# Kernel optimization log

Measured on AMD Instinct MI355X. Metric: run time of the kernel, lower is better.

The kernel has to match this reference:

```python
import jax, jax.numpy as jnp
import numpy as np

K = 7  # local_kernel_size


def conv2d(x, w, b, pad):
    # x: [B,C,H,W], w: [O,I,kh,kw]
    y = jax.lax.conv_general_dilated(
        x, w, window_strides=(1, 1), padding=[(pad, pad), (pad, pad)],
        dimension_numbers=("NCHW", "OIHW", "NCHW"))
    return y + b[None, :, None, None]


def kernel_normalize(kernel, k):
    # kernel: [B, k*k, H, W]; zero-mean over tap dim, then add 1/(k*k)
    km = jnp.mean(kernel, axis=1, keepdims=True)
    return kernel - km + 1.0 / (k * k)


def local_conv_feat(img, kernel, k):
    # Fused dynamic local conv: avoids materializing [B,C,k*k,H,W].
    # Tap order matches F.unfold row-major (dy, dx).
    B, C, H, W = img.shape
    pad = (k - 1) // 2
    imgp = jnp.pad(img, ((0, 0), (0, 0), (pad, pad), (pad, pad)))
    out = jnp.zeros_like(img)
    for dy in range(k):
        for dx in range(k):
            idx = dy * k + dx
            out = out + imgp[:, :, dy:dy + H, dx:dx + W] * kernel[:, idx:idx + 1]
    return out


def setup_inputs() -> dict:
    key = jax.random.key(0)
    ks = jax.random.split(key, 14)
    B, C, H, W = 4, 64, 128, 128
    w = lambda k, shape: jax.random.normal(k, shape, jnp.float32) * 0.05
    return {
        "x": jax.random.normal(ks[0], (B, C, H, W), jnp.float32),
        "kernel_features": jax.random.normal(ks[1], (B, C, H, W), jnp.float32),
        # feature_path: two 3x3 convs
        "fw1": w(ks[2], (C, C, 3, 3)), "fb1": jnp.zeros((C,), jnp.float32),
        "fw2": w(ks[3], (C, C, 3, 3)), "fb2": jnp.zeros((C,), jnp.float32),
        # multiplicative_path: two 3x3 convs
        "mw1": w(ks[4], (C, C, 3, 3)), "mb1": jnp.zeros((C,), jnp.float32),
        "mw2": w(ks[5], (C, C, 3, 3)), "mb2": jnp.zeros((C,), jnp.float32),
        # local_filter_path: two 1x1 convs, last outputs k*k channels
        "lw1": w(ks[6], (C, C, 1, 1)), "lb1": jnp.zeros((C,), jnp.float32),
        "lw2": w(ks[7], (K * K, C, 1, 1)), "lb2": jnp.zeros((K * K,), jnp.float32),
    }


def reference(x, kernel_features, fw1, fb1, fw2, fb2, mw1, mb1, mw2, mb2, lw1, lb1, lw2, lb2):
    # feature_path: ReLU -> conv3x3 -> ReLU -> conv3x3
    fp = conv2d(jax.nn.relu(conv2d(jax.nn.relu(x), fw1, fb1, 1)), fw2, fb2, 1)
    # multiplicative_path: conv3x3 -> ReLU -> conv3x3
    mp = conv2d(jax.nn.relu(conv2d(kernel_features, mw1, mb1, 1)), mw2, mb2, 1)
    # local_filter_path: conv1x1 -> ReLU -> conv1x1 (-> k*k channels)
    lp = conv2d(jax.nn.relu(conv2d(kernel_features, lw1, lb1, 0)), lw2, lb2, 0)
    lp = kernel_normalize(lp, K)
    feat = fp * mp
    filtered = local_conv_feat(feat, lp, K)
    return x + filtered
```

## Files before the change

kernel.cpp:

```cpp
#include <hip/hip_runtime.h>
#include <hip/hip_bf16.h>

#define Cc 64
#define Hc 128
#define Wc 128
#define HWc (Hc * Wc)
#define Bc 4

typedef __attribute__((ext_vector_type(8))) short short8;
typedef __attribute__((ext_vector_type(4))) float float4v;

static __device__ __forceinline__ unsigned short f2bu(float f) {
    __hip_bfloat16 h = __float2bfloat16(f);
    return *(unsigned short*)&h;
}
static __device__ __forceinline__ float bulo(unsigned int u) {
    return __uint_as_float((u & 0xffffu) << 16);
}
static __device__ __forceinline__ float buhi(unsigned int u) {
    return __uint_as_float(u & 0xffff0000u);
}

static __device__ __forceinline__ void gl_lds16(const void* g, void* l) {
    __builtin_amdgcn_global_load_lds(
        (const __attribute__((address_space(1))) unsigned int*)g,
        (__attribute__((address_space(3))) unsigned int*)l, 16, 0, 0);
}

__global__ __launch_bounds__(256) void prep_k(
    const float* __restrict__ x, const float* __restrict__ kf,
    const float* __restrict__ fw1, const float* __restrict__ fw2,
    const float* __restrict__ mw1, const float* __restrict__ mw2,
    const float* __restrict__ lw1, const float* __restrict__ lw2,
    unsigned short* __restrict__ xb, unsigned short* __restrict__ kfb,
    unsigned short* __restrict__ wbase, unsigned short* __restrict__ zpage)
{
    const int bid = blockIdx.x;
    const int tid = threadIdx.x;

    if (bid < 512) {
        const bool isx = bid < 256;
        const float* src = isx ? x : kf;
        unsigned short* dst = isx ? xb : kfb;
        const int px = (isx ? bid : bid - 256) * 256 + tid;
        const int b  = px >> 14;
        const int hw = px & 16383;
        const float* s = src + (size_t)b * Cc * HWc + hw;
        unsigned short* d = dst + (size_t)px * Cc;
#pragma unroll
        for (int c8 = 0; c8 < 8; ++c8) {
            unsigned int pk[4];
#pragma unroll
            for (int jp = 0; jp < 4; ++jp) {
                float v0 = s[(size_t)(c8 * 8 + jp * 2 + 0) * HWc];
                float v1 = s[(size_t)(c8 * 8 + jp * 2 + 1) * HWc];
                if (isx) { v0 = fmaxf(v0, 0.f); v1 = fmaxf(v1, 0.f); }
                pk[jp] = (unsigned int)f2bu(v0) | ((unsigned int)f2bu(v1) << 16);
            }
            *(uint4*)(d + c8 * 8) = make_uint4(pk[0], pk[1], pk[2], pk[3]);
        }
    } else if (bid < 584) {
        const int wbid  = bid - 512;
        const int which = wbid / 18;
        const float* w = (which == 0) ? fw1 : (which == 1) ? fw2 : (which == 2) ? mw1 : mw2;
        unsigned short* wb = wbase + (size_t)which * 36864;
        const int g = (wbid % 18) * 256 + tid;
        if (g >= 4608) return;
        const int lane = g & 63;
        const int smt  = g >> 6;
        const int s    = smt >> 2;
        const int mt   = smt & 3;
        const int co   = mt * 16 + (lane & 15);
        const int kb   = s * 32 + (lane >> 4) * 8;
        unsigned int pk[4];
#pragma unroll
        for (int jp = 0; jp < 4; ++jp) {
            int k0 = kb + jp * 2, k1 = k0 + 1;
            float v0 = w[((size_t)co * Cc + (k0 & 63)) * 9 + (k0 >> 6)];
            float v1 = w[((size_t)co * Cc + (k1 & 63)) * 9 + (k1 >> 6)];
            pk[jp] = (unsigned int)f2bu(v0) | ((unsigned int)f2bu(v1) << 16);
        }
        *(uint4*)(wb + (size_t)g * 8) = make_uint4(pk[0], pk[1], pk[2], pk[3]);
    } else if (bid < 588) {
        const int wbid  = bid - 584;
        const int which = wbid >> 1;
        const float* w = which ? lw2 : lw1;
        const int Cout = which ? 49 : 64;
        unsigned short* wb = wbase + 4 * 36864 + (size_t)which * 4096;
        const int g = (wbid & 1) * 256 + tid;
        const int lane = g & 63;
        const int smt  = g >> 6;
        const int s    = smt >> 2;
        const int mt   = smt & 3;
        const int co   = mt * 16 + (lane & 15);
        const int kb   = s * 32 + (lane >> 4) * 8;
        unsigned int pk[4];
#pragma unroll
        for (int jp = 0; jp < 4; ++jp) {
            int k0 = kb + jp * 2, k1 = k0 + 1;
            float v0 = (co < Cout) ? w[(size_t)co * Cc + k0] : 0.f;
            float v1 = (co < Cout) ? w[(size_t)co * Cc + k1] : 0.f;
            pk[jp] = (unsigned int)f2bu(v0) | ((unsigned int)f2bu(v1) << 16);
        }
        *(uint4*)(wb + (size_t)g * 8) = make_uint4(pk[0], pk[1], pk[2], pk[3]);
    } else {
        if (tid < 64) ((unsigned int*)zpage)[tid] = 0;
    }
}

#define STAGE_DMA(INPTR, SBUF)                                                \
    for (int k = wv; k < 33; k += 4) {                                        \
        const int u_  = k * 8 + (lane >> 3);                                  \
        const int j_  = lane & 7;                                             \
        const int r_  = u_ / 66;                                              \
        const int c_  = u_ - r_ * 66;                                         \
        const int gh_ = h0 - 1 + r_;                                          \
        const int gw_ = w0 - 1 + c_;                                          \
        const bool ok_ = ((unsigned)gh_ < (unsigned)Hc) && ((unsigned)gw_ < (unsigned)Wc); \
        const int ch_ = j_ ^ (u_ & 7);                                        \
        const unsigned short* g_ = ok_                                        \
            ? (INPTR) + ((((size_t)b * Hc + gh_) * Wc + gw_) << 6) + (ch_ << 3) \
            : zpage + (ch_ << 3);                                             \
        gl_lds16(g_, &(SBUF)[k * 512]);                                       \
    }

#define LOAD_A(W, s, m) (*(const short8*)((W) + (size_t)(s) * 2048 + (size_t)(m) * 512))
#define LOAD_B(SB, s, nt) ({                                                  \
        const int tap_ = (s) >> 1;                                            \
        const int qb_  = rowb[tap_ / 3] + tap_ % 3;                           \
        const int ch0_ = ((s) & 1) * 4 + quad;                                \
        *(const short8*)&(SB)[(qb_ + (nt) * 16) * 64 + ((ch0_ ^ (qb_ & 7)) << 3)]; })

#define CONV_GEMM(APTR, ACC, SB)                                              \
    {                                                                         \
        short8 a_buf[4][2], b_cur[4], b_nxt[4];                               \
        _Pragma("unroll")                                                     \
        for (int q = 0; q < 3; ++q)                                           \
            _Pragma("unroll")                                                 \
            for (int m = 0; m < 2; ++m) a_buf[q][m] = LOAD_A(APTR, q, m);     \
        _Pragma("unroll")                                                     \
        for (int nt = 0; nt < 4; ++nt) b_cur[nt] = LOAD_B(SB, 0, nt);         \
        _Pragma("unroll")                                                     \
        for (int s = 0; s < 18; ++s) {                                        \
            if (s + 3 < 18) {                                                 \
                _Pragma("unroll")                                             \
                for (int m = 0; m < 2; ++m)                                   \
                    a_buf[(s + 3) & 3][m] = LOAD_A(APTR, s + 3, m);           \
            }                                                                 \
            if (s + 1 < 18) {                                                 \
                _Pragma("unroll")                                             \
                for (int nt = 0; nt < 4; ++nt)                                \
                    b_nxt[nt] = LOAD_B(SB, s + 1, nt);                        \
            }                                                                 \
            _Pragma("unroll")                                                 \
            for (int nt = 0; nt < 4; ++nt)                                    \
                _Pragma("unroll")                                             \
                for (int m = 0; m < 2; ++m)                                   \
                    ACC[m][nt] = __builtin_amdgcn_mfma_f32_16x16x32_bf16(     \
                        a_buf[s & 3][m], b_cur[nt], ACC[m][nt], 0, 0, 0);     \
            if (s + 1 < 18) {                                                 \
                _Pragma("unroll")                                             \
                for (int nt = 0; nt < 4; ++nt) b_cur[nt] = b_nxt[nt];         \
            }                                                                 \
        }                                                                     \
    }

__global__ __launch_bounds__(256) void conv1_lp_k(
    const unsigned short* __restrict__ in0,
    const unsigned short* __restrict__ in1,
    const unsigned short* __restrict__ wfrag0,
    const unsigned short* __restrict__ wfrag1,
    const float* __restrict__ bias0,
    const float* __restrict__ bias1,
    const unsigned short* __restrict__ zpage,
    unsigned short* __restrict__ out0,
    unsigned short* __restrict__ out1,
    const unsigned short* __restrict__ w1, const float* __restrict__ b1,
    const unsigned short* __restrict__ w2, const float* __restrict__ b2,
    unsigned short* __restrict__ lpout)
{
    __shared__ unsigned short s_b[264 * 64];

    const int tid  = threadIdx.x;
    const int lane = tid & 63;
    const int wv   = tid >> 6;
    const int quad = lane >> 4;
    const int glin = blockIdx.x;
    const int xcd  = glin & 7;
    const int slot = glin >> 3;

    if (slot < 128) {
        const int sel = slot >> 6;
        const int hti = slot & 63;
        const int b   = xcd >> 1;
        const int w0  = (xcd & 1) * 64;
        const int h0  = hti * 2;

        const unsigned short* in    = sel ? in1 : in0;
        const unsigned short* wfrag = sel ? wfrag1 : wfrag0;
        const float*          bias  = sel ? bias1 : bias0;
        unsigned short*       out   = sel ? out1 : out0;

        STAGE_DMA(in, s_b);
        __syncthreads();

        const int rowsel = wv >> 1;
        const int cohalf = wv & 1;
        const int n15    = lane & 15;
        const unsigned short* aptr = wfrag + (((size_t)(cohalf * 2) * 64 + lane) << 3);

        int rowb[3];
#pragma unroll
        for (int ky = 0; ky < 3; ++ky) rowb[ky] = (rowsel + ky) * 66 + n15;

        float4v acc[2][4];
#pragma unroll
        for (int m = 0; m < 2; ++m)
#pragma unroll
            for (int nt = 0; nt < 4; ++nt) acc[m][nt] = (float4v){0.f, 0.f, 0.f, 0.f};

        CONV_GEMM(aptr, acc, s_b);

        const int h = h0 + rowsel;
#pragma unroll
        for (int m = 0; m < 2; ++m) {
            const int mt  = cohalf * 2 + m;
            const int co0 = mt * 16 + quad * 4;
            float4 bv = *(const float4*)&bias[co0];
#pragma unroll
            for (int nt = 0; nt < 4; ++nt) {
                const size_t pix = ((size_t)b * Hc + h) * Wc + w0 + nt * 16 + n15;
                ushort4 pk;
                pk.x = f2bu(fmaxf(acc[m][nt][0] + bv.x, 0.f));
                pk.y = f2bu(fmaxf(acc[m][nt][1] + bv.y, 0.f));
                pk.z = f2bu(fmaxf(acc[m][nt][2] + bv.z, 0.f));
                pk.w = f2bu(fmaxf(acc[m][nt][3] + bv.w, 0.f));
                *(ushort4*)&out[pix * Cc + co0] = pk;
            }
        }
    } else {
        const int lpid = xcd * 128 + (slot - 128);
        const int p    = lane & 15;
        const size_t pix = (size_t)lpid * 64 + wv * 16 + p;
        unsigned short* st = &s_b[wv * 1024];

        float4v acc1[4];
#pragma unroll
        for (int mt = 0; mt < 4; ++mt) acc1[mt] = (float4v){0.f, 0.f, 0.f, 0.f};
#pragma unroll
        for (int s = 0; s < 2; ++s) {
            short8 bfr = *(const short8*)&in1[pix * Cc + s * 32 + quad * 8];
#pragma unroll
            for (int mt = 0; mt < 4; ++mt) {
                short8 afr = *(const short8*)&w1[(size_t)(((s * 4 + mt) << 6) + lane) << 3];
                acc1[mt] = __builtin_amdgcn_mfma_f32_16x16x32_bf16(afr, bfr, acc1[mt], 0, 0, 0);
            }
        }

#pragma unroll
        for (int mt = 0; mt < 4; ++mt) {
            const int co0 = mt * 16 + quad * 4;
            float4 bv = *(const float4*)&b1[co0];
            ushort4 pk;
            pk.x = f2bu(fmaxf(acc1[mt][0] + bv.x, 0.f));
            pk.y = f2bu(fmaxf(acc1[mt][1] + bv.y, 0.f));
            pk.z = f2bu(fmaxf(acc1[mt][2] + bv.z, 0.f));
            pk.w = f2bu(fmaxf(acc1[mt][3] + bv.w, 0.f));
            const int cg = co0 >> 3;
            *(ushort4*)&st[p * 64 + ((cg ^ (p & 7)) << 3) + (quad & 1) * 4] = pk;
        }
        __syncthreads();

        float4v acc2[4];
#pragma unroll
        for (int mt = 0; mt < 4; ++mt) acc2[mt] = (float4v){0.f, 0.f, 0.f, 0.f};
#pragma unroll
        for (int s = 0; s < 2; ++s) {
            const int cg = s * 4 + quad;
            short8 bfr = *(const short8*)&st[p * 64 + ((cg ^ (p & 7)) << 3)];
#pragma unroll
            for (int mt = 0; mt < 4; ++mt) {
                short8 afr = *(const short8*)&w2[(size_t)(((s * 4 + mt) << 6) + lane) << 3];
                acc2[mt] = __builtin_amdgcn_mfma_f32_16x16x32_bf16(afr, bfr, acc2[mt], 0, 0, 0);
            }
        }

        float v[4][4];
        float partial = 0.f;
#pragma unroll
        for (int mt = 0; mt < 4; ++mt) {
#pragma unroll
            for (int r = 0; r < 4; ++r) {
                const int tap = mt * 16 + quad * 4 + r;
                float val = (tap < 49) ? (acc2[mt][r] + b2[tap]) : 0.f;
                v[mt][r] = val;
                partial += val;
            }
        }
        partial += __shfl_xor(partial, 16, 64);
        partial += __shfl_xor(partial, 32, 64);
        const float m = partial * (1.f / 49.f) - (1.f / 49.f);

        const int b  = (int)(pix >> 14);
        const int hw = (int)(pix & 16383);
#pragma unroll
        for (int mt = 0; mt < 4; ++mt) {
#pragma unroll
            for (int r = 0; r < 4; ++r) {
                const int tap = mt * 16 + quad * 4 + r;
                if (tap < 49)
                    lpout[((size_t)b * 49 + tap) * HWc + hw] = f2bu(v[mt][r] - m);
            }
        }
    }
}

__global__ __launch_bounds__(256) void conv2_fused_k(
    const unsigned short* __restrict__ t1f,
    const unsigned short* __restrict__ t1m,
    const unsigned short* __restrict__ wf,
    const unsigned short* __restrict__ wm,
    const float* __restrict__ bf,
    const float* __restrict__ bm,
    const unsigned short* __restrict__ zpage,
    unsigned short* __restrict__ featp)
{
    __shared__ unsigned short s_b2[2][264 * 64];

    const int tid  = threadIdx.x;
    const int lane = tid & 63;
    const int wv   = tid >> 6;
    const int glin = blockIdx.x;
    const int xcd  = glin & 7;
    const int slot = glin >> 3;
    const int b    = xcd >> 1;
    const int w0   = (xcd & 1) * 64;
    const int h0   = slot * 2;

    STAGE_DMA(t1f, s_b2[0]);
    STAGE_DMA(t1m, s_b2[1]);
    __syncthreads();

    const int rowsel = wv >> 1;
    const int cohalf = wv & 1;
    const int quad   = lane >> 4;
    const int n15    = lane & 15;

    int rowb[3];
#pragma unroll
    for (int ky = 0; ky < 3; ++ky) rowb[ky] = (rowsel + ky) * 66 + n15;

    float4v acc[2][4];
#pragma unroll
    for (int m = 0; m < 2; ++m)
#pragma unroll
        for (int nt = 0; nt < 4; ++nt) acc[m][nt] = (float4v){0.f, 0.f, 0.f, 0.f};

    {
        const unsigned short* aptr = wf + (((size_t)(cohalf * 2) * 64 + lane) << 3);
        CONV_GEMM(aptr, acc, s_b2[0]);
    }

    float fpv[2][4][4];
#pragma unroll
    for (int m = 0; m < 2; ++m) {
        const int mt  = cohalf * 2 + m;
        const int co0 = mt * 16 + quad * 4;
        float4 bv = *(const float4*)&bf[co0];
#pragma unroll
        for (int nt = 0; nt < 4; ++nt) {
            fpv[m][nt][0] = bulo((unsigned int)f2bu(acc[m][nt][0] + bv.x));
            fpv[m][nt][1] = bulo((unsigned int)f2bu(acc[m][nt][1] + bv.y));
            fpv[m][nt][2] = bulo((unsigned int)f2bu(acc[m][nt][2] + bv.z));
            fpv[m][nt][3] = bulo((unsigned int)f2bu(acc[m][nt][3] + bv.w));
        }
    }

#pragma unroll
    for (int m = 0; m < 2; ++m)
#pragma unroll
        for (int nt = 0; nt < 4; ++nt) acc[m][nt] = (float4v){0.f, 0.f, 0.f, 0.f};

    {
        const unsigned short* aptr = wm + (((size_t)(cohalf * 2) * 64 + lane) << 3);
        CONV_GEMM(aptr, acc, s_b2[1]);
    }

    const int h = h0 + rowsel;
#pragma unroll
    for (int m = 0; m < 2; ++m) {
        const int mt  = cohalf * 2 + m;
        const int co0 = mt * 16 + quad * 4;
        float4 bv = *(const float4*)&bm[co0];
#pragma unroll
        for (int nt = 0; nt < 4; ++nt) {
            const int px = h * Wc + w0 + nt * 16 + n15;
            float v[4] = {acc[m][nt][0] + bv.x, acc[m][nt][1] + bv.y,
                          acc[m][nt][2] + bv.z, acc[m][nt][3] + bv.w};
#pragma unroll
            for (int r = 0; r < 4; ++r)
                featp[((size_t)b * Cc + co0 + r) * HWc + px] =
                    f2bu(v[r] * fpv[m][nt][r]);
        }
    }
}

__global__ __launch_bounds__(256) void local_conv_v4(
    const float* __restrict__ x, const unsigned short* __restrict__ featp,
    const unsigned short* __restrict__ lp, float* __restrict__ out)
{
    const int tid  = threadIdx.x;
    const int glin = blockIdx.x;
    const int xcd  = glin & 7;
    const int slot = glin >> 3;
    const int pair = xcd * 8 + (slot >> 4);
    const int cg   = slot & 15;
    const int b    = pair >> 4;
    const int hti  = pair & 15;

    const int w4  = (tid & 31) * 4;
    const int ro  = tid >> 5;
    const int h   = hti * 8 + ro;
    const int c0  = cg * 4;

    float msk[12];
#pragma unroll
    for (int e = 0; e < 12; ++e) {
        int gw = w4 - 4 + e;
        msk[e] = ((unsigned)gw < (unsigned)Wc) ? 1.f : 0.f;
    }

    float acc[4][4];
#pragma unroll
    for (int ch = 0; ch < 4; ++ch)
#pragma unroll
        for (int p = 0; p < 4; ++p) acc[ch][p] = 0.f;

    const unsigned short* lpb = lp + (size_t)b * 49 * HWc + (size_t)h * Wc + w4;
    const unsigned short* fb  = featp + ((size_t)b * Cc + c0) * HWc;

#pragma unroll
    for (int dy = 0; dy < 7; ++dy) {
        const int gh = h + dy - 3;
        if ((unsigned)gh >= (unsigned)Hc) continue;

        float lpf[7][4];
#pragma unroll
        for (int dx = 0; dx < 7; ++dx) {
            uint2 lv = *(const uint2*)&lpb[(size_t)(dy * 7 + dx) * HWc];
            lpf[dx][0] = bulo(lv.x); lpf[dx][1] = buhi(lv.x);
            lpf[dx][2] = bulo(lv.y); lpf[dx][3] = buhi(lv.y);
        }

        const unsigned short* frow = fb + (size_t)gh * Wc + w4;
#pragma unroll
        for (int ch = 0; ch < 4; ++ch) {
            const unsigned short* fr = frow + (size_t)ch * HWc;
            uint2 a  = *(const uint2*)(fr - 4);
            uint2 bq = *(const uint2*)(fr);
            uint2 cq = *(const uint2*)(fr + 4);
            float f[12];
            f[0]  = bulo(a.x);             f[1]  = buhi(a.x) * msk[1];
            f[2]  = bulo(a.y) * msk[2];    f[3]  = buhi(a.y) * msk[3];
            f[4]  = bulo(bq.x);            f[5]  = buhi(bq.x);
            f[6]  = bulo(bq.y);            f[7]  = buhi(bq.y);
            f[8]  = bulo(cq.x) * msk[8];   f[9]  = buhi(cq.x) * msk[9];
            f[10] = bulo(cq.y) * msk[10];  f[11] = buhi(cq.y);
#pragma unroll
            for (int dx = 0; dx < 7; ++dx)
#pragma unroll
                for (int p = 0; p < 4; ++p)
                    acc[ch][p] = fmaf(f[p + dx + 1], lpf[dx][p], acc[ch][p]);
        }
    }

#pragma unroll
    for (int ch = 0; ch < 4; ++ch) {
        const size_t idx = ((size_t)b * Cc + c0 + ch) * HWc + (size_t)h * Wc + w4;
        float4 xv = *(const float4*)&x[idx];
        float4 r  = {acc[ch][0] + xv.x, acc[ch][1] + xv.y,
                     acc[ch][2] + xv.z, acc[ch][3] + xv.w};
        *(float4*)&out[idx] = r;
    }
}

extern "C" void kernel_launch(void* const* d_in, const int* in_sizes, int n_in,
                              void* d_out, int out_size, void* d_ws, size_t ws_size,
                              hipStream_t stream)
{
    const float* x   = (const float*)d_in[0];
    const float* kf  = (const float*)d_in[1];
    const float* fw1 = (const float*)d_in[2];
    const float* fb1 = (const float*)d_in[3];
    const float* fw2 = (const float*)d_in[4];
    const float* fb2 = (const float*)d_in[5];
    const float* mw1 = (const float*)d_in[6];
    const float* mb1 = (const float*)d_in[7];
    const float* mw2 = (const float*)d_in[8];
    const float* mb2 = (const float*)d_in[9];
    const float* lw1 = (const float*)d_in[10];
    const float* lb1 = (const float*)d_in[11];
    const float* lw2 = (const float*)d_in[12];
    const float* lb2 = (const float*)d_in[13];

    float* out = (float*)d_out;
    char*  ws  = (char*)d_ws;

    const size_t NBH = (size_t)Bc * HWc * Cc * 2;
    const size_t LPH = (size_t)Bc * 49 * HWc * 2;
    const size_t WBA = (size_t)(4 * 36864 + 2 * 4096) * 2;

    unsigned short* t1f   = (unsigned short*)(ws);
    unsigned short* t1m   = (unsigned short*)(ws + NBH);
    unsigned short* featp = (unsigned short*)(ws + 2 * NBH);
    unsigned short* lpb   = (unsigned short*)(ws + 3 * NBH);
    unsigned short* xb    = (unsigned short*)(ws + 3 * NBH + LPH);
    unsigned short* kfb   = (unsigned short*)((char*)xb + NBH);
    unsigned short* wbase = (unsigned short*)((char*)kfb + NBH);
    unsigned short* zpage = (unsigned short*)((char*)wbase + WBA);
    unsigned short* wb1   = wbase;
    unsigned short* wb2   = wbase + 36864;
    unsigned short* wb3   = wbase + 2 * 36864;
    unsigned short* wb4   = wbase + 3 * 36864;
    unsigned short* wl1   = wbase + 4 * 36864;
    unsigned short* wl2   = wbase + 4 * 36864 + 4096;

    dim3 blk(256);

    prep_k<<<dim3(589), blk, 0, stream>>>(x, kf, fw1, fw2, mw1, mw2, lw1, lw2,
                                          xb, kfb, wbase, zpage);

    conv1_lp_k<<<dim3(2048), blk, 0, stream>>>(xb, kfb, wb1, wb3, fb1, mb1, zpage,
                                               t1f, t1m, wl1, lb1, wl2, lb2, lpb);

    conv2_fused_k<<<dim3(512), blk, 0, stream>>>(t1f, t1m, wb2, wb4, fb2, mb2,
                                                 zpage, featp);

    local_conv_v4<<<dim3(1024), blk, 0, stream>>>(x, featp, lpb, out);
}
```

Before: 161.6 us.

## Fuse all four stages into one persistent kernel with grid barriers

Replaces the four separate launches (prep, conv1+local-filter, conv2+multiply, local conv) with a single 512-block persistent kernel that separates the phases with atomic-counter grid barriers. Each block now does both conv1 branches with two LDS buffers, plus two local-filter tiles and two local-conv tiles. The aim is to remove launch gaps and kernel-boundary drains. In exchange it adds spin-wait barriers that need all blocks co-resident, uses fewer blocks per phase, and holds larger LDS per block, which may lower occupancy.

```diff
diff --git a/kernel.cpp b/kernel.cpp
--- a/kernel.cpp
+++ b/kernel.cpp
@@ -25,87 +25,6 @@
     __builtin_amdgcn_global_load_lds(
         (const __attribute__((address_space(1))) unsigned int*)g,
         (__attribute__((address_space(3))) unsigned int*)l, 16, 0, 0);
-}
-
-__global__ __launch_bounds__(256) void prep_k(
-    const float* __restrict__ x, const float* __restrict__ kf,
-    const float* __restrict__ fw1, const float* __restrict__ fw2,
-    const float* __restrict__ mw1, const float* __restrict__ mw2,
-    const float* __restrict__ lw1, const float* __restrict__ lw2,
-    unsigned short* __restrict__ xb, unsigned short* __restrict__ kfb,
-    unsigned short* __restrict__ wbase, unsigned short* __restrict__ zpage)
-{
-    const int bid = blockIdx.x;
-    const int tid = threadIdx.x;
-
-    if (bid < 512) {
-        const bool isx = bid < 256;
-        const float* src = isx ? x : kf;
-        unsigned short* dst = isx ? xb : kfb;
-        const int px = (isx ? bid : bid - 256) * 256 + tid;
-        const int b  = px >> 14;
-        const int hw = px & 16383;
-        const float* s = src + (size_t)b * Cc * HWc + hw;
-        unsigned short* d = dst + (size_t)px * Cc;
-#pragma unroll
-        for (int c8 = 0; c8 < 8; ++c8) {
-            unsigned int pk[4];
-#pragma unroll
-            for (int jp = 0; jp < 4; ++jp) {
-                float v0 = s[(size_t)(c8 * 8 + jp * 2 + 0) * HWc];
-                float v1 = s[(size_t)(c8 * 8 + jp * 2 + 1) * HWc];
-                if (isx) { v0 = fmaxf(v0, 0.f); v1 = fmaxf(v1, 0.f); }
-                pk[jp] = (unsigned int)f2bu(v0) | ((unsigned int)f2bu(v1) << 16);
-            }
-            *(uint4*)(d + c8 * 8) = make_uint4(pk[0], pk[1], pk[2], pk[3]);
-        }
-    } else if (bid < 584) {
-        const int wbid  = bid - 512;
-        const int which = wbid / 18;
-        const float* w = (which == 0) ? fw1 : (which == 1) ? fw2 : (which == 2) ? mw1 : mw2;
-        unsigned short* wb = wbase + (size_t)which * 36864;
-        const int g = (wbid % 18) * 256 + tid;
-        if (g >= 4608) return;
-        const int lane = g & 63;
-        const int smt  = g >> 6;
-        const int s    = smt >> 2;
-        const int mt   = smt & 3;
-        const int co   = mt * 16 + (lane & 15);
-        const int kb   = s * 32 + (lane >> 4) * 8;
-        unsigned int pk[4];
-#pragma unroll
-        for (int jp = 0; jp < 4; ++jp) {
-            int k0 = kb + jp * 2, k1 = k0 + 1;
-            float v0 = w[((size_t)co * Cc + (k0 & 63)) * 9 + (k0 >> 6)];
-            float v1 = w[((size_t)co * Cc + (k1 & 63)) * 9 + (k1 >> 6)];
-            pk[jp] = (unsigned int)f2bu(v0) | ((unsigned int)f2bu(v1) << 16);
-        }
-        *(uint4*)(wb + (size_t)g * 8) = make_uint4(pk[0], pk[1], pk[2], pk[3]);
-    } else if (bid < 588) {
-        const int wbid  = bid - 584;
-        const int which = wbid >> 1;
-        const float* w = which ? lw2 : lw1;
-        const int Cout = which ? 49 : 64;
-        unsigned short* wb = wbase + 4 * 36864 + (size_t)which * 4096;
-        const int g = (wbid & 1) * 256 + tid;
-        const int lane = g & 63;
-        const int smt  = g >> 6;
-        const int s    = smt >> 2;
-        const int mt   = smt & 3;
-        const int co   = mt * 16 + (lane & 15);
-        const int kb   = s * 32 + (lane >> 4) * 8;
-        unsigned int pk[4];
-#pragma unroll
-        for (int jp = 0; jp < 4; ++jp) {
-            int k0 = kb + jp * 2, k1 = k0 + 1;
-            float v0 = (co < Cout) ? w[(size_t)co * Cc + k0] : 0.f;
-            float v1 = (co < Cout) ? w[(size_t)co * Cc + k1] : 0.f;
-            pk[jp] = (unsigned int)f2bu(v0) | ((unsigned int)f2bu(v1) << 16);
-        }
-        *(uint4*)(wb + (size_t)g * 8) = make_uint4(pk[0], pk[1], pk[2], pk[3]);
-    } else {
-        if (tid < 64) ((unsigned int*)zpage)[tid] = 0;
-    }
 }
 
 #define STAGE_DMA(INPTR, SBUF)                                                \
@@ -165,322 +84,405 @@
         }                                                                     \
     }
 
-__global__ __launch_bounds__(256) void conv1_lp_k(
-    const unsigned short* __restrict__ in0,
-    const unsigned short* __restrict__ in1,
-    const unsigned short* __restrict__ wfrag0,
-    const unsigned short* __restrict__ wfrag1,
-    const float* __restrict__ bias0,
-    const float* __restrict__ bias1,
-    const unsigned short* __restrict__ zpage,
-    unsigned short* __restrict__ out0,
-    unsigned short* __restrict__ out1,
-    const unsigned short* __restrict__ w1, const float* __restrict__ b1,
-    const unsigned short* __restrict__ w2, const float* __restrict__ b2,
-    unsigned short* __restrict__ lpout)
+#define CONV1_EPI(ACC, BIASP, OUTP)                                           \
+    _Pragma("unroll")                                                         \
+    for (int m = 0; m < 2; ++m) {                                             \
+        const int mt_  = cohalf * 2 + m;                                      \
+        const int co0_ = mt_ * 16 + quad * 4;                                 \
+        float4 bv_ = *(const float4*)&(BIASP)[co0_];                          \
+        _Pragma("unroll")                                                     \
+        for (int nt = 0; nt < 4; ++nt) {                                      \
+            const size_t pix_ = ((size_t)b * Hc + h) * Wc + w0 + nt * 16 + n15; \
+            ushort4 pk_;                                                      \
+            pk_.x = f2bu(fmaxf((ACC)[m][nt][0] + bv_.x, 0.f));                \
+            pk_.y = f2bu(fmaxf((ACC)[m][nt][1] + bv_.y, 0.f));                \
+            pk_.z = f2bu(fmaxf((ACC)[m][nt][2] + bv_.z, 0.f));                \
+            pk_.w = f2bu(fmaxf((ACC)[m][nt][3] + bv_.w, 0.f));                \
+            *(ushort4*)&(OUTP)[pix_ * Cc + co0_] = pk_;                       \
+        }                                                                     \
+    }
+
+static __device__ __forceinline__ void grid_bar(unsigned int* syncc, int idx) {
+    __syncthreads();
+    if (threadIdx.x == 0) {
+        __threadfence();
+        unsigned int* c = syncc + idx * 64;
+        atomicAdd(c, 1u);
+        int guard = 0;
+        while (atomicAdd(c, 0u) < gridDim.x && ++guard < (1 << 22))
+            __builtin_amdgcn_s_sleep(2);
+        __threadfence();
+    }
+    __syncthreads();
+}
+
+__global__ __launch_bounds__(256, 2) void fused_all(
+    const float* __restrict__ x, const float* __restrict__ kf,
+    const float* __restrict__ fw1, const float* __restrict__ fw2,
+    const float* __restrict__ mw1, const float* __restrict__ mw2,
+    const float* __restrict__ lw1, const float* __restrict__ lw2,
+    const float* __restrict__ fb1, const float* __restrict__ mb1,
+    const float* __restrict__ fb2, const float* __restrict__ mb2,
+    const float* __restrict__ lb1, const float* __restrict__ lb2,
+    unsigned short* __restrict__ xb, unsigned short* __restrict__ kfb,
+    unsigned short* __restrict__ wbase, unsigned short* __restrict__ zpage,
+    unsigned short* __restrict__ t1f, unsigned short* __restrict__ t1m,
+    unsigned short* __restrict__ featp, unsigned short* __restrict__ lpb,
+    float* __restrict__ out, unsigned int* __restrict__ syncc)
 {
-    __shared__ unsigned short s_b[264 * 64];
+    __shared__ unsigned short s_b2[2][264 * 64];
 
     const int tid  = threadIdx.x;
     const int lane = tid & 63;
     const int wv   = tid >> 6;
     const int quad = lane >> 4;
-    const int glin = blockIdx.x;
-    const int xcd  = glin & 7;
-    const int slot = glin >> 3;
-
-    if (slot < 128) {
-        const int sel = slot >> 6;
-        const int hti = slot & 63;
+    const int bid  = blockIdx.x;
+
+    const unsigned short* wb1 = wbase;
+    const unsigned short* wb2 = wbase + 36864;
+    const unsigned short* wb3 = wbase + 2 * 36864;
+    const unsigned short* wb4 = wbase + 3 * 36864;
+    const unsigned short* wl1 = wbase + 4 * 36864;
+    const unsigned short* wl2 = wbase + 4 * 36864 + 4096;
+
+    {
+        const bool isx = bid < 256;
+        const float* src = isx ? x : kf;
+        unsigned short* dst = isx ? xb : kfb;
+        const int px = (bid & 255) * 256 + tid;
+        const int b  = px >> 14;
+        const int hw = px & 16383;
+        const float* s = src + (size_t)b * Cc * HWc + hw;
+        unsigned short* d = dst + (size_t)px * Cc;
+#pragma unroll
+        for (int c8 = 0; c8 < 8; ++c8) {
+            unsigned int pk[4];
+#pragma unroll
+            for (int jp = 0; jp < 4; ++jp) {
+                float v0 = s[(size_t)(c8 * 8 + jp * 2 + 0) * HWc];
+                float v1 = s[(size_t)(c8 * 8 + jp * 2 + 1) * HWc];
+                if (isx) { v0 = fmaxf(v0, 0.f); v1 = fmaxf(v1, 0.f); }
+                pk[jp] = (unsigned int)f2bu(v0) | ((unsigned int)f2bu(v1) << 16);
+            }
+            *(uint4*)(d + c8 * 8) = make_uint4(pk[0], pk[1], pk[2], pk[3]);
+        }
+
+        if (bid < 72) {
+            const int which = bid / 18;
+            const float* w = (which == 0) ? fw1 : (which == 1) ? fw2 : (which == 2) ? mw1 : mw2;
+            unsigned short* wb = wbase + (size_t)which * 36864;
+            const int g   = (bid % 18) * 256 + tid;
+            const int gl  = g & 63;
+            const int smt = g >> 6;
+            const int sS  = smt >> 2;
+            const int mt  = smt & 3;
+            const int co  = mt * 16 + (gl & 15);
+            const int kb  = sS * 32 + (gl >> 4) * 8;
+            unsigned int pk[4];
+#pragma unroll
+            for (int jp = 0; jp < 4; ++jp) {
+                int k0 = kb + jp * 2, k1 = k0 + 1;
+                float v0 = w[((size_t)co * Cc + (k0 & 63)) * 9 + (k0 >> 6)];
+                float v1 = w[((size_t)co * Cc + (k1 & 63)) * 9 + (k1 >> 6)];
+                pk[jp] = (unsigned int)f2bu(v0) | ((unsigned int)f2bu(v1) << 16);
+            }
+            *(uint4*)(wb + (size_t)g * 8) = make_uint4(pk[0], pk[1], pk[2], pk[3]);
+        } else if (bid < 76) {
+            const int wbid  = bid - 72;
+            const int which = wbid >> 1;
+            const float* w  = which ? lw2 : lw1;
+            const int Cout  = which ? 49 : 64;
+            unsigned short* wb = wbase + 4 * 36864 + (size_t)which * 4096;
+            const int g   = (wbid & 1) * 256 + tid;
+            const int gl  = g & 63;
+            const int smt = g >> 6;
+            const int sS  = smt >> 2;
+            const int mt  = smt & 3;
+            const int co  = mt * 16 + (gl & 15);
+            const int kb  = sS * 32 + (gl >> 4) * 8;
+            unsigned int pk[4];
+#pragma unroll
+            for (int jp = 0; jp < 4; ++jp) {
+                int k0 = kb + jp * 2, k1 = k0 + 1;
+                float v0 = (co < Cout) ? w[(size_t)co * Cc + k0] : 0.f;
+                float v1 = (co < Cout) ? w[(size_t)co * Cc + k1] : 0.f;
+                pk[jp] = (unsigned int)f2bu(v0) | ((unsigned int)f2bu(v1) << 16);
+            }
+            *(uint4*)(wb + (size_t)g * 8) = make_uint4(pk[0], pk[1], pk[2], pk[3]);
+        } else if (bid == 76) {
+            if (tid < 64) ((unsigned int*)zpage)[tid] = 0;
+        }
+    }
+    grid_bar(syncc, 0);
+
+    {
+        const int xcd = bid & 7;
+        const int sl  = bid >> 3;
         const int b   = xcd >> 1;
         const int w0  = (xcd & 1) * 64;
-        const int h0  = hti * 2;
-
-        const unsigned short* in    = sel ? in1 : in0;
-        const unsigned short* wfrag = sel ? wfrag1 : wfrag0;
-        const float*          bias  = sel ? bias1 : bias0;
-        unsigned short*       out   = sel ? out1 : out0;
-
-        STAGE_DMA(in, s_b);
+        const int h0  = sl * 2;
+
+        STAGE_DMA(xb,  s_b2[0]);
+        STAGE_DMA(kfb, s_b2[1]);
         __syncthreads();
 
         const int rowsel = wv >> 1;
         const int cohalf = wv & 1;
         const int n15    = lane & 15;
-        const unsigned short* aptr = wfrag + (((size_t)(cohalf * 2) * 64 + lane) << 3);
+        const int h      = h0 + rowsel;
 
         int rowb[3];
 #pragma unroll
         for (int ky = 0; ky < 3; ++ky) rowb[ky] = (rowsel + ky) * 66 + n15;
 
+        {
+            float4v acc[2][4];
+#pragma unroll
+            for (int m = 0; m < 2; ++m)
+#pragma unroll
+                for (int nt = 0; nt < 4; ++nt) acc[m][nt] = (float4v){0.f, 0.f, 0.f, 0.f};
+            const unsigned short* aptr = wb1 + (((size_t)(cohalf * 2) * 64 + lane) << 3);
+            CONV_GEMM(aptr, acc, s_b2[0]);
+            CONV1_EPI(acc, fb1, t1f);
+        }
+        {
+            float4v acc[2][4];
+#pragma unroll
+            for (int m = 0; m < 2; ++m)
+#pragma unroll
+                for (int nt = 0; nt < 4; ++nt) acc[m][nt] = (float4v){0.f, 0.f, 0.f, 0.f};
+            const unsigned short* aptr = wb3 + (((size_t)(cohalf * 2) * 64 + lane) << 3);
+            CONV_GEMM(aptr, acc, s_b2[1]);
+            CONV1_EPI(acc, mb1, t1m);
+        }
+        __syncthreads();
+
+        for (int ui = 0; ui < 2; ++ui) {
+            const int lpid = xcd * 128 + ui * 64 + sl;
+            const int p = lane & 15;
+            const size_t pix = (size_t)lpid * 64 + wv * 16 + p;
+            unsigned short* st = &s_b2[0][(size_t)(ui * 4 + wv) * 1024];
+
+            float4v acc1[4];
+#pragma unroll
+            for (int mt = 0; mt < 4; ++mt) acc1[mt] = (float4v){0.f, 0.f, 0.f, 0.f};
+#pragma unroll
+            for (int s = 0; s < 2; ++s) {
+                short8 bfr = *(const short8*)&kfb[pix * Cc + s * 32 + quad * 8];
+#pragma unroll
+                for (int mt = 0; mt < 4; ++mt) {
+                    short8 afr = *(const short8*)&wl1[(size_t)(((s * 4 + mt) << 6) + lane) << 3];
+                    acc1[mt] = __builtin_amdgcn_mfma_f32_16x16x32_bf16(afr, bfr, acc1[mt], 0, 0, 0);
+                }
+            }
+
+#pragma unroll
+            for (int mt = 0; mt < 4; ++mt) {
+                const int co0 = mt * 16 + quad * 4;
+                float4 bv = *(const float4*)&lb1[co0];
+                ushort4 pk;
+                pk.x = f2bu(fmaxf(acc1[mt][0] + bv.x, 0.f));
+                pk.y = f2bu(fmaxf(acc1[mt][1] + bv.y, 0.f));
+                pk.z = f2bu(fmaxf(acc1[mt][2] + bv.z, 0.f));
+                pk.w = f2bu(fmaxf(acc1[mt][3] + bv.w, 0.f));
+                const int cg = co0 >> 3;
+                *(ushort4*)&st[p * 64 + ((cg ^ (p & 7)) << 3) + (quad & 1) * 4] = pk;
+            }
+            __syncthreads();
+
+            float4v acc2[4];
+#pragma unroll
+            for (int mt = 0; mt < 4; ++mt) acc2[mt] = (float4v){0.f, 0.f, 0.f, 0.f};
+#pragma unroll
+            for (int s = 0; s < 2; ++s) {
+                const int cg = s * 4 + quad;
+                short8 bfr = *(const short8*)&st[p * 64 + ((cg ^ (p & 7)) << 3)];
+#pragma unroll
+                for (int mt = 0; mt < 4; ++mt) {
+                    short8 afr = *(const short8*)&wl2[(size_t)(((s * 4 + mt) << 6) + lane) << 3];
+                    acc2[mt] = __builtin_amdgcn_mfma_f32_16x16x32_bf16(afr, bfr, acc2[mt], 0, 0, 0);
+                }
+            }
+
+            float v[4][4];
+            float partial = 0.f;
+#pragma unroll
+            for (int mt = 0; mt < 4; ++mt) {
+#pragma unroll
+                for (int r = 0; r < 4; ++r) {
+                    const int tap = mt * 16 + quad * 4 + r;
+                    float val = (tap < 49) ? (acc2[mt][r] + lb2[tap]) : 0.f;
+                    v[mt][r] = val;
+                    partial += val;
+                }
+            }
+            partial += __shfl_xor(partial, 16, 64);
+            partial += __shfl_xor(partial, 32, 64);
+            const float mval = partial * (1.f / 49.f) - (1.f / 49.f);
+
+            const int bI = (int)(pix >> 14);
+            const int hw = (int)(pix & 16383);
+#pragma unroll
+            for (int mt = 0; mt < 4; ++mt) {
+#pragma unroll
+                for (int r = 0; r < 4; ++r) {
+                    const int tap = mt * 16 + quad * 4 + r;
+                    if (tap < 49)
+                        lpb[((size_t)bI * 49 + tap) * HWc + hw] = f2bu(v[mt][r] - mval);
+                }
+            }
+        }
+    }
+    grid_bar(syncc, 1);
+
+    {
+        const int xcd = bid & 7;
+        const int sl  = bid >> 3;
+        const int b   = xcd >> 1;
+        const int w0  = (xcd & 1) * 64;
+        const int h0  = sl * 2;
+
+        STAGE_DMA(t1f, s_b2[0]);
+        STAGE_DMA(t1m, s_b2[1]);
+        __syncthreads();
+
+        const int rowsel = wv >> 1;
+        const int cohalf = wv & 1;
+        const int n15    = lane & 15;
+
+        int rowb[3];
+#pragma unroll
+        for (int ky = 0; ky < 3; ++ky) rowb[ky] = (rowsel + ky) * 66 + n15;
+
         float4v acc[2][4];
 #pragma unroll
         for (int m = 0; m < 2; ++m)
 #pragma unroll
             for (int nt = 0; nt < 4; ++nt) acc[m][nt] = (float4v){0.f, 0.f, 0.f, 0.f};
 
-        CONV_GEMM(aptr, acc, s_b);
-
-        const int h = h0 + rowsel;
+        {
+            const unsigned short* aptr = wb2 + (((size_t)(cohalf * 2) * 64 + lane) << 3);
+            CONV_GEMM(aptr, acc, s_b2[0]);
+        }
+
+        float fpv[2][4][4];
 #pragma unroll
         for (int m = 0; m < 2; ++m) {
             const int mt  = cohalf * 2 + m;
             const int co0 = mt * 16 + quad * 4;
-            float4 bv = *(const float4*)&bias[co0];
+            float4 bv = *(const float4*)&fb2[co0];
 #pragma unroll
             for (int nt = 0; nt < 4; ++nt) {
-                const size_t pix = ((size_t)b * Hc + h) * Wc + w0 + nt * 16 + n15;
-                ushort4 pk;
-                pk.x = f2bu(fmaxf(acc[m][nt][0] + bv.x, 0.f));
-                pk.y = f2bu(fmaxf(acc[m][nt][1] + bv.y, 0.f));
-                pk.z = f2bu(fmaxf(acc[m][nt][2] + bv.z, 0.f));
-                pk.w = f2bu(fmaxf(acc[m][nt][3] + bv.w, 0.f));
-                *(ushort4*)&out[pix * Cc + co0] = pk;
-            }
-        }
-    } else {
-        const int lpid = xcd * 128 + (slot - 128);
-        const int p    = lane & 15;
-        const size_t pix = (size_t)lpid * 64 + wv * 16 + p;
-        unsigned short* st = &s_b[wv * 1024];
-
-        float4v acc1[4];
-#pragma unroll
-        for (int mt = 0; mt < 4; ++mt) acc1[mt] = (float4v){0.f, 0.f, 0.f, 0.f};
-#pragma unroll
-        for (int s = 0; s < 2; ++s) {
-            short8 bfr = *(const short8*)&in1[pix * Cc + s * 32 + quad * 8];
-#pragma unroll
-            for (int mt = 0; mt < 4; ++mt) {
-                short8 afr = *(const short8*)&w1[(size_t)(((s * 4 + mt) << 6) + lane) << 3];
-                acc1[mt] = __builtin_amdgcn_mfma_f32_16x16x32_bf16(afr, bfr, acc1[mt], 0, 0, 0);
-            }
-        }
-
-#pragma unroll
-        for (int mt = 0; mt < 4; ++mt) {
+                fpv[m][nt][0] = bulo((unsigned int)f2bu(acc[m][nt][0] + bv.x));
+                fpv[m][nt][1] = bulo((unsigned int)f2bu(acc[m][nt][1] + bv.y));
+                fpv[m][nt][2] = bulo((unsigned int)f2bu(acc[m][nt][2] + bv.z));
+                fpv[m][nt][3] = bulo((unsigned int)f2bu(acc[m][nt][3] + bv.w));
+            }
+        }
+
+#pragma unroll
+        for (int m = 0; m < 2; ++m)
+#pragma unroll
+            for (int nt = 0; nt < 4; ++nt) acc[m][nt] = (float4v){0.f, 0.f, 0.f, 0.f};
+
+        {
+            const unsigned short* aptr = wb4 + (((size_t)(cohalf * 2) * 64 + lane) << 3);
+            CONV_GEMM(aptr, acc, s_b2[1]);
+        }
+
+        const int h = h0 + rowsel;
+#pragma unroll
+        for (int m = 0; m < 2; ++m) {
+            const int mt  = cohalf * 2 + m;
             const int co0 = mt * 16 + quad * 4;
-            float4 bv = *(const float4*)&b1[co0];
-            ushort4 pk;
-            pk.x = f2bu(fmaxf(acc1[mt][0] + bv.x, 0.f));
-            pk.y = f2bu(fmaxf(acc1[mt][1] + bv.y, 0.f));
-            pk.z = f2bu(fmaxf(acc1[mt][2] + bv.z, 0.f));
-            pk.w = f2bu(fmaxf(acc1[mt][3] + bv.w, 0.f));
-            const int cg = co0 >> 3;
-            *(ushort4*)&st[p * 64 + ((cg ^ (p & 7)) << 3) + (quad & 1) * 4] = pk;
-        }
-        __syncthreads();
-
-        float4v acc2[4];
-#pragma unroll
-        for (int mt = 0; mt < 4; ++mt) acc2[mt] = (float4v){0.f, 0.f, 0.f, 0.f};
-#pragma unroll
-        for (int s = 0; s < 2; ++s) {
-            const int cg = s * 4 + quad;
-            short8 bfr = *(const short8*)&st[p * 64 + ((cg ^ (p & 7)) << 3)];
-#pragma unroll
-            for (int mt = 0; mt < 4; ++mt) {
-                short8 afr = *(const short8*)&w2[(size_t)(((s * 4 + mt) << 6) + lane) << 3];
-                acc2[mt] = __builtin_amdgcn_mfma_f32_16x16x32_bf16(afr, bfr, acc2[mt], 0, 0, 0);
-            }
-        }
-
-        float v[4][4];
-        float partial = 0.f;
-#pragma unroll
-        for (int mt = 0; mt < 4; ++mt) {
-#pragma unroll
-            for (int r = 0; r < 4; ++r) {
-                const int tap = mt * 16 + quad * 4 + r;
-                float val = (tap < 49) ? (acc2[mt][r] + b2[tap]) : 0.f;
-                v[mt][r] = val;
-                partial += val;
-            }
-        }
-        partial += __shfl_xor(partial, 16, 64);
-        partial += __shfl_xor(partial, 32, 64);
-        const float m = partial * (1.f / 49.f) - (1.f / 49.f);
-
-        const int b  = (int)(pix >> 14);
-        const int hw = (int)(pix & 16383);
-#pragma unroll
-        for (int mt = 0; mt < 4; ++mt) {
-#pragma unroll
-            for (int r = 0; r < 4; ++r) {
-                const int tap = mt * 16 + quad * 4 + r;
-                if (tap < 49)
-                    lpout[((size_t)b * 49 + tap) * HWc + hw] = f2bu(v[mt][r] - m);
-            }
-        }
-    }
-}
-
-__global__ __launch_bounds__(256) void conv2_fused_k(
-    const unsigned short* __restrict__ t1f,
-    const unsigned short* __restrict__ t1m,
-    const unsigned short* __restrict__ wf,
-    const unsigned short* __restrict__ wm,
-    const float* __restrict__ bf,
-    const float* __restrict__ bm,
-    const unsigned short* __restrict__ zpage,
-    unsigned short* __restrict__ featp)
-{
-    __shared__ unsigned short s_b2[2][264 * 64];
-
-    const int tid  = threadIdx.x;
-    const int lane = tid & 63;
-    const int wv   = tid >> 6;
-    const int glin = blockIdx.x;
-    const int xcd  = glin & 7;
-    const int slot = glin >> 3;
-    const int b    = xcd >> 1;
-    const int w0   = (xcd & 1) * 64;
-    const int h0   = slot * 2;
-
-    STAGE_DMA(t1f, s_b2[0]);
-    STAGE_DMA(t1m, s_b2[1]);
-    __syncthreads();
-
-    const int rowsel = wv >> 1;
-    const int cohalf = wv & 1;
-    const int quad   = lane >> 4;
-    const int n15    = lane & 15;
-
-    int rowb[3];
-#pragma unroll
-    for (int ky = 0; ky < 3; ++ky) rowb[ky] = (rowsel + ky) * 66 + n15;
-
-    float4v acc[2][4];
-#pragma unroll
-    for (int m = 0; m < 2; ++m)
-#pragma unroll
-        for (int nt = 0; nt < 4; ++nt) acc[m][nt] = (float4v){0.f, 0.f, 0.f, 0.f};
-
-    {
-        const unsigned short* aptr = wf + (((size_t)(cohalf * 2) * 64 + lane) << 3);
-        CONV_GEMM(aptr, acc, s_b2[0]);
-    }
-
-    float fpv[2][4][4];
-#pragma unroll
-    for (int m = 0; m < 2; ++m) {
-        const int mt  = cohalf * 2 + m;
-        const int co0 = mt * 16 + quad * 4;
-        float4 bv = *(const float4*)&bf[co0];
-#pragma unroll
-        for (int nt = 0; nt < 4; ++nt) {
-            fpv[m][nt][0] = bulo((unsigned int)f2bu(acc[m][nt][0] + bv.x));
-            fpv[m][nt][1] = bulo((unsigned int)f2bu(acc[m][nt][1] + bv.y));
-            fpv[m][nt][2] = bulo((unsigned int)f2bu(acc[m][nt][2] + bv.z));
-            fpv[m][nt][3] = bulo((unsigned int)f2bu(acc[m][nt][3] + bv.w));
-        }
-    }
-
-#pragma unroll
-    for (int m = 0; m < 2; ++m)
-#pragma unroll
-        for (int nt = 0; nt < 4; ++nt) acc[m][nt] = (float4v){0.f, 0.f, 0.f, 0.f};
-
-    {
-        const unsigned short* aptr = wm + (((size_t)(cohalf * 2) * 64 + lane) << 3);
-        CONV_GEMM(aptr, acc, s_b2[1]);
-    }
-
-    const int h = h0 + rowsel;
-#pragma unroll
-    for (int m = 0; m < 2; ++m) {
-        const int mt  = cohalf * 2 + m;
-        const int co0 = mt * 16 + quad * 4;
-        float4 bv = *(const float4*)&bm[co0];
-#pragma unroll
-        for (int nt = 0; nt < 4; ++nt) {
-            const int px = h * Wc + w0 + nt * 16 + n15;
-            float v[4] = {acc[m][nt][0] + bv.x, acc[m][nt][1] + bv.y,
-                          acc[m][nt][2] + bv.z, acc[m][nt][3] + bv.w};
-#pragma unroll
-            for (int r = 0; r < 4; ++r)
-                featp[((size_t)b * Cc + co0 + r) * HWc + px] =
-                    f2bu(v[r] * fpv[m][nt][r]);
-        }
-    }
-}
-
-__global__ __launch_bounds__(256) void local_conv_v4(
-    const float* __restrict__ x, const unsigned short* __restrict__ featp,
-    const unsigned short* __restrict__ lp, float* __restrict__ out)
-{
-    const int tid  = threadIdx.x;
-    const int glin = blockIdx.x;
-    const int xcd  = glin & 7;
-    const int slot = glin >> 3;
-    const int pair = xcd * 8 + (slot >> 4);
-    const int cg   = slot & 15;
-    const int b    = pair >> 4;
-    const int hti  = pair & 15;
-
-    const int w4  = (tid & 31) * 4;
-    const int ro  = tid >> 5;
-    const int h   = hti * 8 + ro;
-    const int c0  = cg * 4;
-
-    float msk[12];
-#pragma unroll
-    for (int e = 0; e < 12; ++e) {
-        int gw = w4 - 4 + e;
-        msk[e] = ((unsigned)gw < (unsigned)Wc) ? 1.f : 0.f;
-    }
-
-    float acc[4][4];
-#pragma unroll
-    for (int ch = 0; ch < 4; ++ch)
-#pragma unroll
-        for (int p = 0; p < 4; ++p) acc[ch][p] = 0.f;
-
-    const unsigned short* lpb = lp + (size_t)b * 49 * HWc + (size_t)h * Wc + w4;
-    const unsigned short* fb  = featp + ((size_t)b * Cc + c0) * HWc;
-
-#pragma unroll
-    for (int dy = 0; dy < 7; ++dy) {
-        const int gh = h + dy - 3;
-        if ((unsigned)gh >= (unsigned)Hc) continue;
-
-        float lpf[7][4];
-#pragma unroll
-        for (int dx = 0; dx < 7; ++dx) {
-            uint2 lv = *(const uint2*)&lpb[(size_t)(dy * 7 + dx) * HWc];
-            lpf[dx][0] = bulo(lv.x); lpf[dx][1] = buhi(lv.x);
-            lpf[dx][2] = bulo(lv.y); lpf[dx][3] = buhi(lv.y);
-        }
-
-        const unsigned short* frow = fb + (size_t)gh * Wc + w4;
+            float4 bv = *(const float4*)&mb2[co0];
+#pragma unroll
+            for (int nt = 0; nt < 4; ++nt) {
+                const int px = h * Wc + w0 + nt * 16 + n15;
+                float v[4] = {acc[m][nt][0] + bv.x, acc[m][nt][1] + bv.y,
+                              acc[m][nt][2] + bv.z, acc[m][nt][3] + bv.w};
+#pragma unroll
+                for (int r = 0; r < 4; ++r)
+                    featp[((size_t)b * Cc + co0 + r) * HWc + px] =
+                        f2bu(v[r] * fpv[m][nt][r]);
+            }
+        }
+    }
+    grid_bar(syncc, 2);
+
+    for (int u = 0; u < 2; ++u) {
+        const int glin = bid + u * 512;
+        const int xcd  = glin & 7;
+        const int slot = glin >> 3;
+        const int pair = xcd * 8 + (slot >> 4);
+        const int cg   = slot & 15;
+        const int b    = pair >> 4;
+        const int hti  = pair & 15;
+
+        const int w4  = (tid & 31) * 4;
+        const int ro  = tid >> 5;
+        const int h   = hti * 8 + ro;
+        const int c0  = cg * 4;
+
+        float msk[12];
+#pragma unroll
+        for (int e = 0; e < 12; ++e) {
+            int gw = w4 - 4 + e;
+            msk[e] = ((unsigned)gw < (unsigned)Wc) ? 1.f : 0.f;
+        }
+
+        float acc[4][4];
+#pragma unroll
+        for (int ch = 0; ch < 4; ++ch)
+#pragma unroll
+            for (int p = 0; p < 4; ++p) acc[ch][p] = 0.f;
+
+        const unsigned short* lpbp = lpb + (size_t)b * 49 * HWc + (size_t)h * Wc + w4;
+        const unsigned short* fb   = featp + ((size_t)b * Cc + c0) * HWc;
+
+#pragma unroll
+        for (int dy = 0; dy < 7; ++dy) {
+            const int gh = h + dy - 3;
+            if ((unsigned)gh >= (unsigned)Hc) continue;
+
+            float lpf[7][4];
+#pragma unroll
+            for (int dx = 0; dx < 7; ++dx) {
+                uint2 lv = *(const uint2*)&lpbp[(size_t)(dy * 7 + dx) * HWc];
+                lpf[dx][0] = bulo(lv.x); lpf[dx][1] = buhi(lv.x);
+                lpf[dx][2] = bulo(lv.y); lpf[dx][3] = buhi(lv.y);
+            }
+
+            const unsigned short* frow = fb + (size_t)gh * Wc + w4;
+#pragma unroll
+            for (int ch = 0; ch < 4; ++ch) {
+                const unsigned short* fr = frow + (size_t)ch * HWc;
+                uint2 a  = *(const uint2*)(fr - 4);
+                uint2 bq = *(const uint2*)(fr);
+                uint2 cq = *(const uint2*)(fr + 4);
+                float f[12];
+                f[0]  = bulo(a.x);             f[1]  = buhi(a.x) * msk[1];
+                f[2]  = bulo(a.y) * msk[2];    f[3]  = buhi(a.y) * msk[3];
+                f[4]  = bulo(bq.x);            f[5]  = buhi(bq.x);
+                f[6]  = bulo(bq.y);            f[7]  = buhi(bq.y);
+                f[8]  = bulo(cq.x) * msk[8];   f[9]  = buhi(cq.x) * msk[9];
+                f[10] = bulo(cq.y) * msk[10];  f[11] = buhi(cq.y);
+#pragma unroll
+                for (int dx = 0; dx < 7; ++dx)
+#pragma unroll
+                    for (int p = 0; p < 4; ++p)
+                        acc[ch][p] = fmaf(f[p + dx + 1], lpf[dx][p], acc[ch][p]);
+            }
+        }
+
 #pragma unroll
         for (int ch = 0; ch < 4; ++ch) {
-            const unsigned short* fr = frow + (size_t)ch * HWc;
-            uint2 a  = *(const uint2*)(fr - 4);
-            uint2 bq = *(const uint2*)(fr);
-            uint2 cq = *(const uint2*)(fr + 4);
-            float f[12];
-            f[0]  = bulo(a.x);             f[1]  = buhi(a.x) * msk[1];
-            f[2]  = bulo(a.y) * msk[2];    f[3]  = buhi(a.y) * msk[3];
-            f[4]  = bulo(bq.x);            f[5]  = buhi(bq.x);
-            f[6]  = bulo(bq.y);            f[7]  = buhi(bq.y);
-            f[8]  = bulo(cq.x) * msk[8];   f[9]  = buhi(cq.x) * msk[9];
-            f[10] = bulo(cq.y) * msk[10];  f[11] = buhi(cq.y);
-#pragma unroll
-            for (int dx = 0; dx < 7; ++dx)
-#pragma unroll
-                for (int p = 0; p < 4; ++p)
-                    acc[ch][p] = fmaf(f[p + dx + 1], lpf[dx][p], acc[ch][p]);
-        }
-    }
-
-#pragma unroll
-    for (int ch = 0; ch < 4; ++ch) {
-        const size_t idx = ((size_t)b * Cc + c0 + ch) * HWc + (size_t)h * Wc + w4;
-        float4 xv = *(const float4*)&x[idx];
-        float4 r  = {acc[ch][0] + xv.x, acc[ch][1] + xv.y,
-                     acc[ch][2] + xv.z, acc[ch][3] + xv.w};
-        *(float4*)&out[idx] = r;
+            const size_t idx = ((size_t)b * Cc + c0 + ch) * HWc + (size_t)h * Wc + w4;
+            float4 xv = *(const float4*)&x[idx];
+            float4 r  = {acc[ch][0] + xv.x, acc[ch][1] + xv.y,
+                         acc[ch][2] + xv.z, acc[ch][3] + xv.w};
+            *(float4*)&out[idx] = r;
+        }
     }
 }
 
@@ -513,28 +515,17 @@
     unsigned short* t1f   = (unsigned short*)(ws);
     unsigned short* t1m   = (unsigned short*)(ws + NBH);
     unsigned short* featp = (unsigned short*)(ws + 2 * NBH);
-    unsigned short* lpb   = (unsigned short*)(ws + 3 * NBH);
+    unsigned short* lpbuf = (unsigned short*)(ws + 3 * NBH);
     unsigned short* xb    = (unsigned short*)(ws + 3 * NBH + LPH);
     unsigned short* kfb   = (unsigned short*)((char*)xb + NBH);
     unsigned short* wbase = (unsigned short*)((char*)kfb + NBH);
     unsigned short* zpage = (unsigned short*)((char*)wbase + WBA);
-    unsigned short* wb1   = wbase;
-    unsigned short* wb2   = wbase + 36864;
-    unsigned short* wb3   = wbase + 2 * 36864;
-    unsigned short* wb4   = wbase + 3 * 36864;
-    unsigned short* wl1   = wbase + 4 * 36864;
-    unsigned short* wl2   = wbase + 4 * 36864 + 4096;
-
-    dim3 blk(256);
-
-    prep_k<<<dim3(589), blk, 0, stream>>>(x, kf, fw1, fw2, mw1, mw2, lw1, lw2,
-                                          xb, kfb, wbase, zpage);
-
-    conv1_lp_k<<<dim3(2048), blk, 0, stream>>>(xb, kfb, wb1, wb3, fb1, mb1, zpage,
-                                               t1f, t1m, wl1, lb1, wl2, lb2, lpb);
-
-    conv2_fused_k<<<dim3(512), blk, 0, stream>>>(t1f, t1m, wb2, wb4, fb2, mb2,
-                                                 zpage, featp);
-
-    local_conv_v4<<<dim3(1024), blk, 0, stream>>>(x, featp, lpb, out);
-}
+    unsigned int*   syncc = (unsigned int*)((char*)zpage + 256);
+
+    hipMemsetAsync(syncc, 0, 3 * 64 * sizeof(unsigned int), stream);
+
+    fused_all<<<dim3(512), dim3(256), 0, stream>>>(
+        x, kf, fw1, fw2, mw1, mw2, lw1, lw2,
+        fb1, mb1, fb2, mb2, lb1, lb2,
+        xb, kfb, wbase, zpage, t1f, t1m, featp, lpbuf, out, syncc);
+}
```

Measured after the change: 342.9 us. 112% more time.
